# Kernel tuning notes

Hardware: AMD Instinct MI355X
Metric: run time of the kernel (lower is better)

Reference implementation:

```python
import jax, jax.numpy as jnp
import numpy as np

N_NODES = 100000
N_EDGES = 1600000
N_GRAPHS = 1024
D = 128
L = 3
BN_EPS = 1e-5


def setup_inputs() -> dict:
    key = jax.random.key(0)
    ks = jax.random.split(key, 16)
    x = jax.random.normal(ks[0], (N_NODES, D), dtype=jnp.float32)
    edge_index = jax.random.randint(ks[1], (2, N_EDGES), 0, N_NODES, dtype=jnp.int64)
    batch = jnp.sort(jax.random.randint(ks[2], (N_NODES,), 0, N_GRAPHS, dtype=jnp.int64))
    w = lambda k, shape: jax.random.normal(k, shape, dtype=jnp.float32) * 0.05
    return {
        "x": x,
        "edge_index": edge_index,
        "batch": batch,
        "conv_W1": w(ks[3], (L, D, D)),
        "conv_b1": w(ks[4], (L, D)),
        "bn_gamma": jax.random.uniform(ks[5], (L, D), dtype=jnp.float32) + 0.5,
        "bn_beta": w(ks[6], (L, D)),
        "bn_mean": w(ks[7], (L, D)),
        "bn_var": jax.random.uniform(ks[8], (L, D), dtype=jnp.float32) + 0.5,
        "conv_W2": w(ks[9], (L, D, D)),
        "conv_b2": w(ks[10], (L, D)),
        "head_W1": w(ks[11], (D, D)),
        "head_b1": w(ks[12], (D,)),
        "head_W2": w(ks[13], (D, D)),
        "head_b2": w(ks[14], (D,)),
    }


def reference(x, edge_index, batch, conv_W1, conv_b1, bn_gamma, bn_beta,
              bn_mean, bn_var, conv_W2, conv_b2, head_W1, head_b1,
              head_W2, head_b2):
    n = x.shape[0]
    src, dst = edge_index[0], edge_index[1]
    for l in range(L):
        # GINConv, eps=0: nn(x + sum_{j->i} x_j)
        agg = jax.ops.segment_sum(x[src], dst, num_segments=n)  # [N, D]
        h = x + agg
        # MLP([in, h, h]): Linear -> BatchNorm(eval) -> ReLU -> Linear
        h = h @ conv_W1[l] + conv_b1[l]
        h = (h - bn_mean[l]) * jax.lax.rsqrt(bn_var[l] + BN_EPS) * bn_gamma[l] + bn_beta[l]
        h = jax.nn.relu(h)
        h = h @ conv_W2[l] + conv_b2[l]
        x = jax.nn.relu(h)  # .relu() in the outer forward
    # global_add_pool over graph ids
    g = jax.ops.segment_sum(x, batch, num_segments=N_GRAPHS)  # [B, D]
    # head MLP (norm=None, dropout inactive at eval): Linear -> ReLU -> Linear
    g = jax.nn.relu(g @ head_W1 + head_b1)
    return g @ head_W2 + head_b2
```

## Files before the change

kernel.cpp:

```cpp
#include <hip/hip_runtime.h>

#define N_NODES  100000
#define N_EDGES  1600000
#define N_GRAPHS 1024
#define D        128
#define BN_EPS   1e-5f

#define FNSLICE      98
#define FSLICE_NODES 1024
#define FSLICE_CAP   20480
#define QCAP         96
#define CCHUNK       4000
#define CGRID        400

typedef short bf16x8 __attribute__((ext_vector_type(8)));
typedef float f32x4  __attribute__((ext_vector_type(4)));

__device__ __forceinline__ ushort f2bf(float f) {
    unsigned int b = __float_as_uint(f);
    return (ushort)((b + 0x7fffu + ((b >> 16) & 1u)) >> 16);
}
__device__ __forceinline__ float bflo(unsigned int u) { return __uint_as_float(u << 16); }
__device__ __forceinline__ float bfhi(unsigned int u) { return __uint_as_float(u & 0xffff0000u); }
__device__ __forceinline__ unsigned int packbf(float x, float y) {
    return (unsigned int)f2bf(x) | ((unsigned int)f2bf(y) << 16);
}


__global__ void zero_kernel(int* __restrict__ p, int n) {
    int i = blockIdx.x * blockDim.x + threadIdx.x;
    if (i < n) p[i] = 0;
}

__global__ __launch_bounds__(256) void compact_kernel(const int* __restrict__ src,
                                                      const int* __restrict__ dst,
                                                      unsigned int* __restrict__ squeue,
                                                      int* __restrict__ slice_tail) {
    __shared__ unsigned int qbuf[FNSLICE * QCAP];
    __shared__ int qcnt[FNSLICE];
    __shared__ int qbase[FNSLICE];
    int t = threadIdx.x;
    for (int i = t; i < FNSLICE; i += 256) qcnt[i] = 0;
    __syncthreads();
    int e0 = blockIdx.x * CCHUNK;
    int eend = e0 + CCHUNK; if (eend > N_EDGES) eend = N_EDGES;
    for (int e = e0 + t; e < eend; e += 256) {
        int d = dst[e], s = src[e];
        int sl = d >> 10;
        unsigned int pk = ((unsigned int)(d & 1023) << 17) | (unsigned int)s;
        int pos = atomicAdd(&qcnt[sl], 1);
        if (pos < QCAP) qbuf[sl * QCAP + pos] = pk;
        else {
            int gp = atomicAdd(&slice_tail[sl], 1);
            squeue[(size_t)sl * FSLICE_CAP + gp] = pk;
        }
    }
    __syncthreads();
    for (int i = t; i < FNSLICE; i += 256) {
        int n = qcnt[i]; if (n > QCAP) n = QCAP;
        qbase[i] = atomicAdd(&slice_tail[i], n);
    }
    __syncthreads();
    int wv = t >> 6, ln = t & 63;
    for (int sl = wv; sl < FNSLICE; sl += 4) {
        int n = qcnt[sl]; if (n > QCAP) n = QCAP;
        int gb = qbase[sl];
        for (int i = ln; i < n; i += 64)
            squeue[(size_t)sl * FSLICE_CAP + gb + i] = qbuf[sl * QCAP + i];
    }
}

__global__ __launch_bounds__(128) void slice_scan(const int* __restrict__ slice_tail,
                                                  int* __restrict__ slice_base,
                                                  int* __restrict__ offsets) {
    __shared__ int part[128];
    int t = threadIdx.x;
    int v = (t < FNSLICE) ? slice_tail[t] : 0;
    part[t] = v;
    __syncthreads();
    for (int off = 1; off < 128; off <<= 1) {
        int u = (t >= off) ? part[t - off] : 0;
        __syncthreads();
        part[t] += u;
        __syncthreads();
    }
    if (t < FNSLICE) slice_base[t] = part[t] - v;
    if (t == 0) offsets[N_NODES] = N_EDGES;
}

__global__ __launch_bounds__(1024) void fill_local(const unsigned int* __restrict__ squeue,
                                                   const int* __restrict__ slice_tail,
                                                   const int* __restrict__ slice_base,
                                                   int* __restrict__ offsets,
                                                   int* __restrict__ csr_src) {
    __shared__ int hist[FSLICE_NODES];
    __shared__ int cur[FSLICE_NODES];
    int sl = blockIdx.x, t = threadIdx.x;
    int n = slice_tail[sl];
    size_t qb = (size_t)sl * FSLICE_CAP;
    int gbase = slice_base[sl];
    hist[t] = 0;
    __syncthreads();
    for (int i = t; i < n; i += 1024)
        atomicAdd(&hist[squeue[qb + i] >> 17], 1);
    __syncthreads();
    int v = hist[t];
    for (int off = 1; off < 1024; off <<= 1) {
        int u = (t >= off) ? hist[t - off] : 0;
        __syncthreads();
        hist[t] += u;
        __syncthreads();
    }
    int excl = hist[t] - v;
    cur[t] = excl;
    int node = sl * FSLICE_NODES + t;
    if (node < N_NODES) offsets[node] = gbase + excl;
    __syncthreads();
    for (int i = t; i < n; i += 1024) {
        unsigned int p = squeue[qb + i];
        int slot = atomicAdd(&cur[p >> 17], 1);
        csr_src[gbase + slot] = (int)(p & 0x1FFFFu);
    }
}

__global__ void gstart_kernel(const int* __restrict__ batch, int* __restrict__ gstart) {
    int g = blockIdx.x * blockDim.x + threadIdx.x;
    if (g > N_GRAPHS) return;
    int lo = 0, hi = N_NODES;
    while (lo < hi) {
        int mid = (lo + hi) >> 1;
        if (batch[mid] < g) lo = mid + 1; else hi = mid;
    }
    gstart[g] = lo;
}


__global__ __launch_bounds__(256) void cvt_x_kernel(const float* __restrict__ x,
                                                    ushort* __restrict__ xb) {
    size_t i = ((size_t)blockIdx.x * 256 + threadIdx.x) * 8;
    float4 v0 = *(const float4*)(x + i);
    float4 v1 = *(const float4*)(x + i + 4);
    uint4 o;
    o.x = packbf(v0.x, v0.y); o.y = packbf(v0.z, v0.w);
    o.z = packbf(v1.x, v1.y); o.w = packbf(v1.z, v1.w);
    *(uint4*)(xb + i) = o;
}

__global__ __launch_bounds__(128) void prep_w_kernel(const float* __restrict__ W1,
                                                     const float* __restrict__ W2,
                                                     ushort* __restrict__ Wt) {
    int i = blockIdx.y, k = blockIdx.x, n = threadIdx.x, l = i >> 1;
    const float* W = (i & 1) ? (W2 + (size_t)l * D * D) : (W1 + (size_t)l * D * D);
    Wt[(size_t)i * D * D + n * D + k] = f2bf(W[k * D + n]);
}

__global__ __launch_bounds__(128) void prep_fold_kernel(
        const float* __restrict__ b1, const float* __restrict__ gamma,
        const float* __restrict__ beta, const float* __restrict__ mean,
        const float* __restrict__ var, const float* __restrict__ b2,
        float* __restrict__ folds) {
    int i = blockIdx.x, j = threadIdx.x, l = i >> 1;
    float s, o;
    if ((i & 1) == 0) {
        float sv = gamma[l * D + j] * rsqrtf(var[l * D + j] + BN_EPS);
        s = sv;
        o = (b1[l * D + j] - mean[l * D + j]) * sv + beta[l * D + j];
    } else {
        s = 1.0f;
        o = b2[l * D + j];
    }
    folds[(size_t)i * 2 * D + j]     = s;
    folds[(size_t)i * 2 * D + D + j] = o;
}

__global__ __launch_bounds__(256) void gather_bf16(const ushort* __restrict__ xb,
                                                   const int* __restrict__ offsets,
                                                   const int* __restrict__ csr_src,
                                                   ushort* __restrict__ hb) {
    int wv = threadIdx.x >> 6, lane = threadIdx.x & 63;
    int node = blockIdx.x * 4 + wv;
    const unsigned int* base = (const unsigned int*)xb;
    unsigned int u = base[(size_t)node * 64 + lane];
    float ax = bflo(u), ay = bfhi(u);
    int b = offsets[node], e = offsets[node + 1];
    int i = b;
    for (; i + 15 < e; i += 16) {
        int s0 = csr_src[i],      s1 = csr_src[i + 1],  s2 = csr_src[i + 2],  s3 = csr_src[i + 3];
        int s4 = csr_src[i + 4],  s5 = csr_src[i + 5],  s6 = csr_src[i + 6],  s7 = csr_src[i + 7];
        int s8 = csr_src[i + 8],  s9 = csr_src[i + 9],  sa = csr_src[i + 10], sb = csr_src[i + 11];
        int sc = csr_src[i + 12], sd = csr_src[i + 13], se = csr_src[i + 14], sf = csr_src[i + 15];
        unsigned int v0 = base[(size_t)s0 * 64 + lane];
        unsigned int v1 = base[(size_t)s1 * 64 + lane];
        unsigned int v2 = base[(size_t)s2 * 64 + lane];
        unsigned int v3 = base[(size_t)s3 * 64 + lane];
        unsigned int v4 = base[(size_t)s4 * 64 + lane];
        unsigned int v5 = base[(size_t)s5 * 64 + lane];
        unsigned int v6 = base[(size_t)s6 * 64 + lane];
        unsigned int v7 = base[(size_t)s7 * 64 + lane];
        unsigned int v8 = base[(size_t)s8 * 64 + lane];
        unsigned int v9 = base[(size_t)s9 * 64 + lane];
        unsigned int va = base[(size_t)sa * 64 + lane];
        unsigned int vb = base[(size_t)sb * 64 + lane];
        unsigned int vc = base[(size_t)sc * 64 + lane];
        unsigned int vd = base[(size_t)sd * 64 + lane];
        unsigned int ve = base[(size_t)se * 64 + lane];
        unsigned int vf = base[(size_t)sf * 64 + lane];
        ax += bflo(v0) + bflo(v1) + bflo(v2) + bflo(v3)
            + bflo(v4) + bflo(v5) + bflo(v6) + bflo(v7)
            + bflo(v8) + bflo(v9) + bflo(va) + bflo(vb)
            + bflo(vc) + bflo(vd) + bflo(ve) + bflo(vf);
        ay += bfhi(v0) + bfhi(v1) + bfhi(v2) + bfhi(v3)
            + bfhi(v4) + bfhi(v5) + bfhi(v6) + bfhi(v7)
            + bfhi(v8) + bfhi(v9) + bfhi(va) + bfhi(vb)
            + bfhi(vc) + bfhi(vd) + bfhi(ve) + bfhi(vf);
    }
    for (; i + 3 < e; i += 4) {
        int s0 = csr_src[i], s1 = csr_src[i + 1], s2 = csr_src[i + 2], s3 = csr_src[i + 3];
        unsigned int v0 = base[(size_t)s0 * 64 + lane];
        unsigned int v1 = base[(size_t)s1 * 64 + lane];
        unsigned int v2 = base[(size_t)s2 * 64 + lane];
        unsigned int v3 = base[(size_t)s3 * 64 + lane];
        ax += bflo(v0) + bflo(v1) + bflo(v2) + bflo(v3);
        ay += bfhi(v0) + bfhi(v1) + bfhi(v2) + bfhi(v3);
    }
    for (; i < e; ++i) {
        unsigned int v = base[(size_t)csr_src[i] * 64 + lane];
        ax += bflo(v); ay += bfhi(v);
    }
    ((unsigned int*)hb)[(size_t)node * 64 + lane] = packbf(ax, ay);
}

__global__ __launch_bounds__(512, 4) void fused_gemm(const ushort* __restrict__ in,
                                                     ushort* __restrict__ out,
                                                     const ushort* __restrict__ Wt1,
                                                     const ushort* __restrict__ Wt2,
                                                     const float* __restrict__ fold1,
                                                     const float* __restrict__ fold2) {
    __shared__ ushort As[128 * 136];
    __shared__ ushort Bs[128 * 136];
    int t = threadIdx.x;
    int row0 = blockIdx.x * 128;

#pragma unroll
    for (int i = 0; i < 4; ++i) {
        int f = t + 512 * i; int m = f >> 4, g = f & 15;
        *(float4*)(As + m * 136 + g * 8) = *(const float4*)(in + (size_t)(row0 + m) * D + g * 8);
        *(float4*)(Bs + m * 136 + g * 8) = *(const float4*)(Wt1 + (size_t)m * D + g * 8);
    }
    __syncthreads();

    int lane = t & 63, wv = t >> 6;
    int quad = lane >> 4, mr = lane & 15;
    int mbase = wv * 16;
    const ushort* ap = As + (mbase + mr) * 136 + quad * 8;
    bf16x8 a0 = *(const bf16x8*)(ap);
    bf16x8 a1 = *(const bf16x8*)(ap + 32);
    bf16x8 a2 = *(const bf16x8*)(ap + 64);
    bf16x8 a3 = *(const bf16x8*)(ap + 96);

#pragma unroll
    for (int nt = 0; nt < 8; ++nt) {
        const ushort* bq = Bs + (nt * 16 + mr) * 136 + quad * 8;
        bf16x8 b0 = *(const bf16x8*)(bq);
        bf16x8 b1 = *(const bf16x8*)(bq + 32);
        bf16x8 b2 = *(const bf16x8*)(bq + 64);
        bf16x8 b3 = *(const bf16x8*)(bq + 96);
        f32x4 acc = {0.f, 0.f, 0.f, 0.f};
        acc = __builtin_amdgcn_mfma_f32_16x16x32_bf16(a0, b0, acc, 0, 0, 0);
        acc = __builtin_amdgcn_mfma_f32_16x16x32_bf16(a1, b1, acc, 0, 0, 0);
        acc = __builtin_amdgcn_mfma_f32_16x16x32_bf16(a2, b2, acc, 0, 0, 0);
        acc = __builtin_amdgcn_mfma_f32_16x16x32_bf16(a3, b3, acc, 0, 0, 0);
        int j = nt * 16 + mr;
        float s = fold1[j], o = fold1[D + j];
#pragma unroll
        for (int r = 0; r < 4; ++r) {
            float z = fmaxf(fmaf(acc[r], s, o), 0.0f);
            As[(mbase + quad * 4 + r) * 136 + j] = f2bf(z);
        }
    }
    __syncthreads();

#pragma unroll
    for (int i = 0; i < 4; ++i) {
        int f = t + 512 * i; int m = f >> 4, g = f & 15;
        *(float4*)(Bs + m * 136 + g * 8) = *(const float4*)(Wt2 + (size_t)m * D + g * 8);
    }
    const ushort* hp = As + (mbase + mr) * 136 + quad * 8;
    bf16x8 h0 = *(const bf16x8*)(hp);
    bf16x8 h1 = *(const bf16x8*)(hp + 32);
    bf16x8 h2 = *(const bf16x8*)(hp + 64);
    bf16x8 h3 = *(const bf16x8*)(hp + 96);
    __syncthreads();

#pragma unroll
    for (int nt = 0; nt < 8; ++nt) {
        const ushort* bq = Bs + (nt * 16 + mr) * 136 + quad * 8;
        bf16x8 b0 = *(const bf16x8*)(bq);
        bf16x8 b1 = *(const bf16x8*)(bq + 32);
        bf16x8 b2 = *(const bf16x8*)(bq + 64);
        bf16x8 b3 = *(const bf16x8*)(bq + 96);
        f32x4 acc = {0.f, 0.f, 0.f, 0.f};
        acc = __builtin_amdgcn_mfma_f32_16x16x32_bf16(h0, b0, acc, 0, 0, 0);
        acc = __builtin_amdgcn_mfma_f32_16x16x32_bf16(h1, b1, acc, 0, 0, 0);
        acc = __builtin_amdgcn_mfma_f32_16x16x32_bf16(h2, b2, acc, 0, 0, 0);
        acc = __builtin_amdgcn_mfma_f32_16x16x32_bf16(h3, b3, acc, 0, 0, 0);
        int j = nt * 16 + mr;
        float o = fold2[D + j];
#pragma unroll
        for (int r = 0; r < 4; ++r) {
            float z = fmaxf(acc[r] + o, 0.0f);
            As[(mbase + quad * 4 + r) * 136 + j] = f2bf(z);
        }
    }
    __syncthreads();

#pragma unroll
    for (int i = 0; i < 8; ++i) {
        int f = t + 512 * i; int lr = f >> 5, g = f & 31;
        if (row0 + lr < N_NODES)
            *(float2*)(out + (size_t)(row0 + lr) * D + g * 4) =
                *(const float2*)(As + lr * 136 + g * 4);
    }
}

__global__ __launch_bounds__(128) void pool_kernel(const ushort* __restrict__ xb,
                                                   const int* __restrict__ gstart,
                                                   float* __restrict__ g) {
    int gr = blockIdx.x, j = threadIdx.x;
    float acc = 0.0f;
    int b = gstart[gr], e = gstart[gr + 1];
    for (int i = b; i < e; ++i)
        acc += __uint_as_float(((unsigned int)xb[(size_t)i * D + j]) << 16);
    g[gr * D + j] = acc;
}

__global__ __launch_bounds__(128) void head_kernel(const float* __restrict__ g,
                                                   const float* __restrict__ W1,
                                                   const float* __restrict__ b1,
                                                   const float* __restrict__ W2,
                                                   const float* __restrict__ b2,
                                                   float* __restrict__ out) {
    __shared__ float row[128];
    __shared__ float t1[128];
    int r = blockIdx.x, j = threadIdx.x;
    row[j] = g[r * D + j];
    __syncthreads();
    float acc = b1[j];
    for (int k = 0; k < D; ++k) acc = fmaf(row[k], W1[k * D + j], acc);
    t1[j] = fmaxf(acc, 0.0f);
    __syncthreads();
    float acc2 = b2[j];
    for (int k = 0; k < D; ++k) acc2 = fmaf(t1[k], W2[k * D + j], acc2);
    out[r * D + j] = acc2;
}

extern "C" void kernel_launch(void* const* d_in, const int* in_sizes, int n_in,
                              void* d_out, int out_size, void* d_ws, size_t ws_size,
                              hipStream_t stream) {
    const float* x        = (const float*)d_in[0];
    const int*   ei       = (const int*)d_in[1];
    const int*   src      = ei;
    const int*   dst      = ei + N_EDGES;
    const int*   batch    = (const int*)d_in[2];
    const float* conv_W1  = (const float*)d_in[3];
    const float* conv_b1  = (const float*)d_in[4];
    const float* bn_gamma = (const float*)d_in[5];
    const float* bn_beta  = (const float*)d_in[6];
    const float* bn_mean  = (const float*)d_in[7];
    const float* bn_var   = (const float*)d_in[8];
    const float* conv_W2  = (const float*)d_in[9];
    const float* conv_b2  = (const float*)d_in[10];
    const float* head_W1  = (const float*)d_in[11];
    const float* head_b1  = (const float*)d_in[12];
    const float* head_W2  = (const float*)d_in[13];
    const float* head_b2  = (const float*)d_in[14];
    float* out = (float*)d_out;

    char* ws = (char*)d_ws;
    size_t off = 0;
    auto alloc = [&](size_t bytes) -> void* {
        void* p = ws + off;
        off = (off + bytes + 255) & ~(size_t)255;
        return p;
    };
    const size_t NODE_BUF = (size_t)(N_NODES + 128) * D * sizeof(ushort);
    ushort* buf0    = (ushort*)alloc(NODE_BUF);
    ushort* buf1    = (ushort*)alloc(NODE_BUF);
    ushort* Wt      = (ushort*)alloc((size_t)6 * D * D * sizeof(ushort));
    float*  folds   = (float*)alloc((size_t)6 * 2 * D * sizeof(float));
    unsigned int* squeue = (unsigned int*)alloc((size_t)FNSLICE * FSLICE_CAP * sizeof(unsigned int));
    int*   csr_src  = (int*)alloc((size_t)N_EDGES * sizeof(int));
    int*   offsets  = (int*)alloc((size_t)(N_NODES + 1) * sizeof(int));
    int*   slice_tail = (int*)alloc((size_t)FNSLICE * sizeof(int));
    int*   slice_base = (int*)alloc((size_t)FNSLICE * sizeof(int));
    int*   gstart   = (int*)alloc((size_t)(N_GRAPHS + 1) * sizeof(int));
    float* gpool    = (float*)alloc((size_t)N_GRAPHS * D * sizeof(float));

    zero_kernel<<<1, 128, 0, stream>>>(slice_tail, FNSLICE);
    compact_kernel<<<CGRID, 256, 0, stream>>>(src, dst, squeue, slice_tail);
    slice_scan<<<1, 128, 0, stream>>>(slice_tail, slice_base, offsets);
    fill_local<<<FNSLICE, 1024, 0, stream>>>(squeue, slice_tail, slice_base,
                                             offsets, csr_src);
    gstart_kernel<<<(N_GRAPHS + 1 + 255) / 256, 256, 0, stream>>>(batch, gstart);
    cvt_x_kernel<<<(N_NODES * D) / (256 * 8), 256, 0, stream>>>(x, buf0);
    prep_w_kernel<<<dim3(128, 6), 128, 0, stream>>>(conv_W1, conv_W2, Wt);
    prep_fold_kernel<<<6, 128, 0, stream>>>(conv_b1, bn_gamma, bn_beta,
                                            bn_mean, bn_var, conv_b2, folds);

    const int FUSED_GRID = (N_NODES + 127) / 128;
    for (int l = 0; l < 3; ++l) {
        gather_bf16<<<N_NODES / 4, 256, 0, stream>>>(buf0, offsets, csr_src, buf1);
        fused_gemm<<<FUSED_GRID, 512, 0, stream>>>(buf1, buf0,
            Wt + (size_t)(2 * l) * D * D, Wt + (size_t)(2 * l + 1) * D * D,
            folds + (size_t)(2 * l) * 2 * D, folds + (size_t)(2 * l + 1) * 2 * D);
    }

    pool_kernel<<<N_GRAPHS, 128, 0, stream>>>(buf0, gstart, gpool);
    head_kernel<<<N_GRAPHS, 128, 0, stream>>>(gpool, head_W1, head_b1,
                                              head_W2, head_b2, out);
}
```

Measured before the change: 457.5 us.

## Merge setup kernels, fold slice scan into fill, fuse pool with head

Five small preprocessing kernels (zeroing, x conversion, weight transpose, BN fold, graph-start search) become one launch with block-range dispatch. The slice prefix scan moves into fill_local, and its node scan now uses wave shuffles instead of a shared-memory Hillis-Steele loop. Pooling and the head MLP are fused into one kernel, and the gather blocks grow from 4 to 16 waves. This cuts launch count and intermediate traffic, but the weight-prep store pattern changes to a strided read and the gather block is larger.

```diff
diff --git a/kernel.cpp b/kernel.cpp
--- a/kernel.cpp
+++ b/kernel.cpp
@@ -13,6 +13,12 @@
 #define CCHUNK       4000
 #define CGRID        400
 
+#define CVT_BLOCKS   6250
+#define PW_BLOCKS    384
+#define FOLD_BLOCKS  3
+#define GST_BLOCKS   5
+#define SETUP_GRID   (CVT_BLOCKS + PW_BLOCKS + FOLD_BLOCKS + GST_BLOCKS + 1)
+
 typedef short bf16x8 __attribute__((ext_vector_type(8)));
 typedef float f32x4  __attribute__((ext_vector_type(4)));
 
@@ -26,10 +32,61 @@
     return (unsigned int)f2bf(x) | ((unsigned int)f2bf(y) << 16);
 }
 
-
-__global__ void zero_kernel(int* __restrict__ p, int n) {
-    int i = blockIdx.x * blockDim.x + threadIdx.x;
-    if (i < n) p[i] = 0;
+__global__ __launch_bounds__(256) void setup_kernel(
+        const float* __restrict__ x, ushort* __restrict__ xb,
+        const float* __restrict__ W1, const float* __restrict__ W2,
+        ushort* __restrict__ Wt,
+        const float* __restrict__ b1, const float* __restrict__ gamma,
+        const float* __restrict__ beta, const float* __restrict__ mean,
+        const float* __restrict__ var, const float* __restrict__ b2,
+        float* __restrict__ folds,
+        const int* __restrict__ batch, int* __restrict__ gstart,
+        int* __restrict__ slice_tail, int* __restrict__ offsets) {
+    int b = blockIdx.x, t = threadIdx.x;
+    if (b < CVT_BLOCKS) {
+        size_t i = ((size_t)b * 256 + t) * 8;
+        float4 v0 = *(const float4*)(x + i);
+        float4 v1 = *(const float4*)(x + i + 4);
+        uint4 o;
+        o.x = packbf(v0.x, v0.y); o.y = packbf(v0.z, v0.w);
+        o.z = packbf(v1.x, v1.y); o.w = packbf(v1.z, v1.w);
+        *(uint4*)(xb + i) = o;
+    } else if (b < CVT_BLOCKS + PW_BLOCKS) {
+        int idx = (b - CVT_BLOCKS) * 256 + t;
+        int i = idx >> 14, r = idx & 16383;
+        int n = r >> 7, k = r & 127, l = i >> 1;
+        const float* W = (i & 1) ? (W2 + (size_t)l * D * D) : (W1 + (size_t)l * D * D);
+        Wt[idx] = f2bf(W[k * D + n]);
+    } else if (b < CVT_BLOCKS + PW_BLOCKS + FOLD_BLOCKS) {
+        int idx = (b - CVT_BLOCKS - PW_BLOCKS) * 256 + t;
+        if (idx < 6 * D) {
+            int i = idx >> 7, j = idx & 127, l = i >> 1;
+            float s, o;
+            if ((i & 1) == 0) {
+                float sv = gamma[l * D + j] * rsqrtf(var[l * D + j] + BN_EPS);
+                s = sv;
+                o = (b1[l * D + j] - mean[l * D + j]) * sv + beta[l * D + j];
+            } else {
+                s = 1.0f;
+                o = b2[l * D + j];
+            }
+            folds[(size_t)i * 2 * D + j]     = s;
+            folds[(size_t)i * 2 * D + D + j] = o;
+        }
+    } else if (b < CVT_BLOCKS + PW_BLOCKS + FOLD_BLOCKS + GST_BLOCKS) {
+        int g = (b - CVT_BLOCKS - PW_BLOCKS - FOLD_BLOCKS) * 256 + t;
+        if (g <= N_GRAPHS) {
+            int lo = 0, hi = N_NODES;
+            while (lo < hi) {
+                int mid = (lo + hi) >> 1;
+                if (batch[mid] < g) lo = mid + 1; else hi = mid;
+            }
+            gstart[g] = lo;
+        }
+    } else {
+        if (t < FNSLICE) slice_tail[t] = 0;
+        if (t == 255) offsets[N_NODES] = N_EDGES;
+    }
 }
 
 __global__ __launch_bounds__(256) void compact_kernel(const int* __restrict__ src,
@@ -70,115 +127,69 @@
     }
 }
 
-__global__ __launch_bounds__(128) void slice_scan(const int* __restrict__ slice_tail,
-                                                  int* __restrict__ slice_base,
-                                                  int* __restrict__ offsets) {
-    __shared__ int part[128];
-    int t = threadIdx.x;
-    int v = (t < FNSLICE) ? slice_tail[t] : 0;
-    part[t] = v;
-    __syncthreads();
-    for (int off = 1; off < 128; off <<= 1) {
-        int u = (t >= off) ? part[t - off] : 0;
-        __syncthreads();
-        part[t] += u;
-        __syncthreads();
-    }
-    if (t < FNSLICE) slice_base[t] = part[t] - v;
-    if (t == 0) offsets[N_NODES] = N_EDGES;
-}
-
 __global__ __launch_bounds__(1024) void fill_local(const unsigned int* __restrict__ squeue,
                                                    const int* __restrict__ slice_tail,
-                                                   const int* __restrict__ slice_base,
                                                    int* __restrict__ offsets,
                                                    int* __restrict__ csr_src) {
     __shared__ int hist[FSLICE_NODES];
     __shared__ int cur[FSLICE_NODES];
+    __shared__ int sbase[128];
+    __shared__ int wsum[16];
     int sl = blockIdx.x, t = threadIdx.x;
     int n = slice_tail[sl];
+    if (t < 128) sbase[t] = (t < FNSLICE) ? slice_tail[t] : 0;
+    hist[t] = 0;
+    __syncthreads();
+    for (int off = 1; off < 128; off <<= 1) {
+        int u = (t < 128 && t >= off) ? sbase[t - off] : 0;
+        __syncthreads();
+        if (t < 128) sbase[t] += u;
+        __syncthreads();
+    }
+    int gbase = (sl == 0) ? 0 : sbase[sl - 1];
     size_t qb = (size_t)sl * FSLICE_CAP;
-    int gbase = slice_base[sl];
-    hist[t] = 0;
-    __syncthreads();
     for (int i = t; i < n; i += 1024)
         atomicAdd(&hist[squeue[qb + i] >> 17], 1);
     __syncthreads();
-    int v = hist[t];
-    for (int off = 1; off < 1024; off <<= 1) {
-        int u = (t >= off) ? hist[t - off] : 0;
-        __syncthreads();
-        hist[t] += u;
-        __syncthreads();
-    }
-    int excl = hist[t] - v;
-    cur[t] = excl;
+    int c = hist[t];
+    int lane = t & 63, w = t >> 6;
+    int sc = c;
+#pragma unroll
+    for (int off = 1; off < 64; off <<= 1) {
+        int u = __shfl_up(sc, off, 64);
+        if (lane >= off) sc += u;
+    }
+    if (lane == 63) wsum[w] = sc;
+    __syncthreads();
+    if (t < 16) {
+        int ws = wsum[t];
+        int s2 = ws;
+#pragma unroll
+        for (int off = 1; off < 16; off <<= 1) {
+            int u = __shfl_up(s2, off, 16);
+            if (t >= off) s2 += u;
+        }
+        wsum[t] = s2 - ws;
+    }
+    __syncthreads();
+    int gslot = gbase + sc + wsum[w] - c;
+    cur[t] = gslot;
     int node = sl * FSLICE_NODES + t;
-    if (node < N_NODES) offsets[node] = gbase + excl;
+    if (node < N_NODES) offsets[node] = gslot;
     __syncthreads();
     for (int i = t; i < n; i += 1024) {
         unsigned int p = squeue[qb + i];
         int slot = atomicAdd(&cur[p >> 17], 1);
-        csr_src[gbase + slot] = (int)(p & 0x1FFFFu);
-    }
-}
-
-__global__ void gstart_kernel(const int* __restrict__ batch, int* __restrict__ gstart) {
-    int g = blockIdx.x * blockDim.x + threadIdx.x;
-    if (g > N_GRAPHS) return;
-    int lo = 0, hi = N_NODES;
-    while (lo < hi) {
-        int mid = (lo + hi) >> 1;
-        if (batch[mid] < g) lo = mid + 1; else hi = mid;
-    }
-    gstart[g] = lo;
-}
-
-
-__global__ __launch_bounds__(256) void cvt_x_kernel(const float* __restrict__ x,
-                                                    ushort* __restrict__ xb) {
-    size_t i = ((size_t)blockIdx.x * 256 + threadIdx.x) * 8;
-    float4 v0 = *(const float4*)(x + i);
-    float4 v1 = *(const float4*)(x + i + 4);
-    uint4 o;
-    o.x = packbf(v0.x, v0.y); o.y = packbf(v0.z, v0.w);
-    o.z = packbf(v1.x, v1.y); o.w = packbf(v1.z, v1.w);
-    *(uint4*)(xb + i) = o;
-}
-
-__global__ __launch_bounds__(128) void prep_w_kernel(const float* __restrict__ W1,
-                                                     const float* __restrict__ W2,
-                                                     ushort* __restrict__ Wt) {
-    int i = blockIdx.y, k = blockIdx.x, n = threadIdx.x, l = i >> 1;
-    const float* W = (i & 1) ? (W2 + (size_t)l * D * D) : (W1 + (size_t)l * D * D);
-    Wt[(size_t)i * D * D + n * D + k] = f2bf(W[k * D + n]);
-}
-
-__global__ __launch_bounds__(128) void prep_fold_kernel(
-        const float* __restrict__ b1, const float* __restrict__ gamma,
-        const float* __restrict__ beta, const float* __restrict__ mean,
-        const float* __restrict__ var, const float* __restrict__ b2,
-        float* __restrict__ folds) {
-    int i = blockIdx.x, j = threadIdx.x, l = i >> 1;
-    float s, o;
-    if ((i & 1) == 0) {
-        float sv = gamma[l * D + j] * rsqrtf(var[l * D + j] + BN_EPS);
-        s = sv;
-        o = (b1[l * D + j] - mean[l * D + j]) * sv + beta[l * D + j];
-    } else {
-        s = 1.0f;
-        o = b2[l * D + j];
-    }
-    folds[(size_t)i * 2 * D + j]     = s;
-    folds[(size_t)i * 2 * D + D + j] = o;
-}
-
-__global__ __launch_bounds__(256) void gather_bf16(const ushort* __restrict__ xb,
-                                                   const int* __restrict__ offsets,
-                                                   const int* __restrict__ csr_src,
-                                                   ushort* __restrict__ hb) {
+        csr_src[slot] = (int)(p & 0x1FFFFu);
+    }
+}
+
+__global__ __launch_bounds__(1024) void gather_bf16(const ushort* __restrict__ xb,
+                                                    const int* __restrict__ offsets,
+                                                    const int* __restrict__ csr_src,
+                                                    ushort* __restrict__ hb) {
     int wv = threadIdx.x >> 6, lane = threadIdx.x & 63;
-    int node = blockIdx.x * 4 + wv;
+    int node = blockIdx.x * 16 + wv;
     const unsigned int* base = (const unsigned int*)xb;
     unsigned int u = base[(size_t)node * 64 + lane];
     float ax = bflo(u), ay = bfhi(u);
@@ -323,35 +334,29 @@
     }
 }
 
-__global__ __launch_bounds__(128) void pool_kernel(const ushort* __restrict__ xb,
-                                                   const int* __restrict__ gstart,
-                                                   float* __restrict__ g) {
-    int gr = blockIdx.x, j = threadIdx.x;
-    float acc = 0.0f;
-    int b = gstart[gr], e = gstart[gr + 1];
-    for (int i = b; i < e; ++i)
-        acc += __uint_as_float(((unsigned int)xb[(size_t)i * D + j]) << 16);
-    g[gr * D + j] = acc;
-}
-
-__global__ __launch_bounds__(128) void head_kernel(const float* __restrict__ g,
-                                                   const float* __restrict__ W1,
-                                                   const float* __restrict__ b1,
-                                                   const float* __restrict__ W2,
-                                                   const float* __restrict__ b2,
-                                                   float* __restrict__ out) {
+__global__ __launch_bounds__(128) void poolhead_kernel(const ushort* __restrict__ xb,
+                                                       const int* __restrict__ gstart,
+                                                       const float* __restrict__ W1,
+                                                       const float* __restrict__ b1,
+                                                       const float* __restrict__ W2,
+                                                       const float* __restrict__ b2,
+                                                       float* __restrict__ out) {
     __shared__ float row[128];
     __shared__ float t1[128];
     int r = blockIdx.x, j = threadIdx.x;
-    row[j] = g[r * D + j];
-    __syncthreads();
-    float acc = b1[j];
-    for (int k = 0; k < D; ++k) acc = fmaf(row[k], W1[k * D + j], acc);
-    t1[j] = fmaxf(acc, 0.0f);
-    __syncthreads();
-    float acc2 = b2[j];
-    for (int k = 0; k < D; ++k) acc2 = fmaf(t1[k], W2[k * D + j], acc2);
-    out[r * D + j] = acc2;
+    float acc = 0.0f;
+    int b = gstart[r], e = gstart[r + 1];
+    for (int i = b; i < e; ++i)
+        acc += __uint_as_float(((unsigned int)xb[(size_t)i * D + j]) << 16);
+    row[j] = acc;
+    __syncthreads();
+    float a1 = b1[j];
+    for (int k = 0; k < D; ++k) a1 = fmaf(row[k], W1[k * D + j], a1);
+    t1[j] = fmaxf(a1, 0.0f);
+    __syncthreads();
+    float a2 = b2[j];
+    for (int k = 0; k < D; ++k) a2 = fmaf(t1[k], W2[k * D + j], a2);
+    out[r * D + j] = a2;
 }
 
 extern "C" void kernel_launch(void* const* d_in, const int* in_sizes, int n_in,
@@ -392,30 +397,23 @@
     int*   csr_src  = (int*)alloc((size_t)N_EDGES * sizeof(int));
     int*   offsets  = (int*)alloc((size_t)(N_NODES + 1) * sizeof(int));
     int*   slice_tail = (int*)alloc((size_t)FNSLICE * sizeof(int));
-    int*   slice_base = (int*)alloc((size_t)FNSLICE * sizeof(int));
     int*   gstart   = (int*)alloc((size_t)(N_GRAPHS + 1) * sizeof(int));
-    float* gpool    = (float*)alloc((size_t)N_GRAPHS * D * sizeof(float));
-
-    zero_kernel<<<1, 128, 0, stream>>>(slice_tail, FNSLICE);
+
+    setup_kernel<<<SETUP_GRID, 256, 0, stream>>>(
+        x, buf0, conv_W1, conv_W2, Wt,
+        conv_b1, bn_gamma, bn_beta, bn_mean, bn_var, conv_b2, folds,
+        batch, gstart, slice_tail, offsets);
     compact_kernel<<<CGRID, 256, 0, stream>>>(src, dst, squeue, slice_tail);
-    slice_scan<<<1, 128, 0, stream>>>(slice_tail, slice_base, offsets);
-    fill_local<<<FNSLICE, 1024, 0, stream>>>(squeue, slice_tail, slice_base,
-                                             offsets, csr_src);
-    gstart_kernel<<<(N_GRAPHS + 1 + 255) / 256, 256, 0, stream>>>(batch, gstart);
-    cvt_x_kernel<<<(N_NODES * D) / (256 * 8), 256, 0, stream>>>(x, buf0);
-    prep_w_kernel<<<dim3(128, 6), 128, 0, stream>>>(conv_W1, conv_W2, Wt);
-    prep_fold_kernel<<<6, 128, 0, stream>>>(conv_b1, bn_gamma, bn_beta,
-                                            bn_mean, bn_var, conv_b2, folds);
+    fill_local<<<FNSLICE, 1024, 0, stream>>>(squeue, slice_tail, offsets, csr_src);
 
     const int FUSED_GRID = (N_NODES + 127) / 128;
     for (int l = 0; l < 3; ++l) {
-        gather_bf16<<<N_NODES / 4, 256, 0, stream>>>(buf0, offsets, csr_src, buf1);
+        gather_bf16<<<N_NODES / 16, 1024, 0, stream>>>(buf0, offsets, csr_src, buf1);
         fused_gemm<<<FUSED_GRID, 512, 0, stream>>>(buf1, buf0,
             Wt + (size_t)(2 * l) * D * D, Wt + (size_t)(2 * l + 1) * D * D,
             folds + (size_t)(2 * l) * 2 * D, folds + (size_t)(2 * l + 1) * 2 * D);
     }
 
-    pool_kernel<<<N_GRAPHS, 128, 0, stream>>>(buf0, gstart, gpool);
-    head_kernel<<<N_GRAPHS, 128, 0, stream>>>(gpool, head_W1, head_b1,
-                                              head_W2, head_b2, out);
-}
+    poolhead_kernel<<<N_GRAPHS, 128, 0, stream>>>(buf0, gstart, head_W1, head_b1,
+                                                  head_W2, head_b2, out);
+}
```

After: 487.3 us. 1.07x slower.
